# Performance work log

Hardware: AMD Instinct MI355X
Metric: run time of the kernel (lower is better)

## Reference

```python
import jax, jax.numpy as jnp
import numpy as np

B, S, D_IN, D_OUT = 4, 2048, 2048, 2048
E, R, TOP_K = 8, 8, 2
ALPHA = 16.0
SCALE = ALPHA / R  # alpha / r


def setup_inputs() -> dict:
    key = jax.random.key(0)
    ks = jax.random.split(key, 6)
    x = jax.random.normal(ks[0], (B, S, D_IN), dtype=jnp.float32)
    # base frozen linear: torch Linear weight [out, in], bias [out]
    W_base = jax.random.normal(ks[1], (D_OUT, D_IN), dtype=jnp.float32) / np.sqrt(D_IN)
    b_base = jax.random.normal(ks[2], (D_OUT,), dtype=jnp.float32) * 0.01
    # router: Linear(in_features, num_experts, bias=False) -> weight [E, in]
    W_router = jax.random.normal(ks[3], (E, D_IN), dtype=jnp.float32) / np.sqrt(D_IN)
    # LoRA experts: A [E, r, in], B [E, out, r] (torch inits B to zero; use small
    # random values so outputs/grads are non-trivial -- math is identical)
    A_w = jax.random.normal(ks[4], (E, R, D_IN), dtype=jnp.float32) / np.sqrt(D_IN)
    B_w = jax.random.normal(ks[5], (E, D_OUT, R), dtype=jnp.float32) * 0.02
    return {"x": x, "W_base": W_base, "b_base": b_base,
            "W_router": W_router, "A_w": A_w, "B_w": B_w}


def reference(x, W_base, b_base, W_router, A_w, B_w):
    # frozen base linear: [B,S,out]
    y = jnp.einsum('bsd,od->bso', x, W_base) + b_base
    # router: logits [B,S,E] -> top-k + softmax over the k selected logits
    logits = jnp.einsum('bsd,ed->bse', x, W_router)
    topk_vals, topk_idx = jax.lax.top_k(logits, TOP_K)       # [B,S,k]
    gates = jax.nn.softmax(topk_vals, axis=-1)               # [B,S,k]
    # all-experts LoRA compute (matches the original dense-stack semantics)
    h = jnp.einsum('bsd,erd->bser', x, A_w)                  # [B,S,E,r]
    expert_outs = jnp.einsum('bser,eor->bseo', h, B_w) * SCALE  # [B,S,E,out]
    # gather the top-k expert outputs and combine with gates
    topk_outs = jnp.take_along_axis(expert_outs, topk_idx[..., None], axis=2)  # [B,S,k,out]
    fused = jnp.sum(topk_outs * gates[..., None], axis=2)    # [B,S,out]
    return y + fused
```

## Files before the change

### kernel.cpp

```cpp
#include <hip/hip_runtime.h>

typedef unsigned short u16;
typedef __attribute__((ext_vector_type(8))) short short8;
typedef __attribute__((ext_vector_type(4))) float f32x4;

#define GLL16(g, l) __builtin_amdgcn_global_load_lds(                         \
    (const __attribute__((address_space(1))) void*)(g),                        \
    (__attribute__((address_space(3))) void*)(l), 16, 0, 0)

__device__ __forceinline__ u16 f2bf(float f) {
  union { float f; unsigned u; } v; v.f = f;
  unsigned u = v.u;
  return (u16)((u + 0x7FFFu + ((u >> 16) & 1u)) >> 16);
}

__global__ __launch_bounds__(512) void k_conv_router(
    const float* __restrict__ x, const float* __restrict__ Wr,
    u16* __restrict__ xbf, float* __restrict__ logits)
{
  __shared__ float wlds[16384];
  {
    const float4* src = (const float4*)Wr;
    float4* dst = (float4*)wlds;
    int t = threadIdx.x;
#pragma unroll
    for (int i = 0; i < 8; ++i) dst[t + i * 512] = src[t + i * 512];
  }
  __syncthreads();
  int wave = threadIdx.x >> 6, lane = threadIdx.x & 63;
  const float4* wv = (const float4*)wlds;
#pragma unroll 1
  for (int s = 0; s < 2; ++s) {
    int tok = blockIdx.x * 16 + wave * 2 + s;
    const float4* xrow = (const float4*)(x + tok * 2048);
    ushort4* orow = (ushort4*)(xbf + tok * 2048);
    float acc[8];
#pragma unroll
    for (int e = 0; e < 8; ++e) acc[e] = 0.f;
#pragma unroll 1
    for (int i = 0; i < 8; ++i) {
      float4 xv = xrow[lane + i * 64];
      ushort4 o;
      o.x = f2bf(xv.x); o.y = f2bf(xv.y);
      o.z = f2bf(xv.z); o.w = f2bf(xv.w);
      orow[lane + i * 64] = o;
#pragma unroll
      for (int e = 0; e < 8; ++e) {
        float4 b = wv[e * 512 + lane + i * 64];
        acc[e] += xv.x * b.x + xv.y * b.y + xv.z * b.z + xv.w * b.w;
      }
    }
#pragma unroll
    for (int e = 0; e < 8; ++e) {
      float v = acc[e];
#pragma unroll
      for (int off = 32; off > 0; off >>= 1) v += __shfl_xor(v, off, 64);
      acc[e] = v;
    }
    if (lane == 0) {
#pragma unroll
      for (int e = 0; e < 8; ++e) logits[tok * 8 + e] = acc[e];
    }
  }
}

__global__ __launch_bounds__(256) void k_convert(
    const float* __restrict__ Wb, const float* __restrict__ Aw,
    const float* __restrict__ Bw,
    u16* __restrict__ wbf, u16* __restrict__ aabf, u16* __restrict__ bmt)
{
  int b = blockIdx.x, t = threadIdx.x;
  if (b < 1024) {
    int tid = b * 256 + t;
    const float4* src = (const float4*)Wb;
    ushort4* dst = (ushort4*)wbf;
#pragma unroll
    for (int i = 0; i < 4; ++i) {
      float4 v = src[tid + i * 262144];
      ushort4 o; o.x = f2bf(v.x); o.y = f2bf(v.y); o.z = f2bf(v.z); o.w = f2bf(v.w);
      dst[tid + i * 262144] = o;
    }
  } else if (b < 1056) {
    int tid = (b - 1024) * 256 + t;
    const float4* src = (const float4*)Aw;
    ushort4* dst = (ushort4*)aabf;
#pragma unroll
    for (int i = 0; i < 4; ++i) {
      float4 v = src[tid + i * 8192];
      ushort4 o; o.x = f2bf(v.x); o.y = f2bf(v.y); o.z = f2bf(v.z); o.w = f2bf(v.w);
      dst[tid + i * 8192] = o;
    }
  } else {
    int n = (b - 1056) * 256 + t;
#pragma unroll
    for (int e = 0; e < 8; ++e) {
      const float4* src = (const float4*)(Bw + e * 16384 + n * 8);
      float4 v0 = src[0], v1 = src[1];
      ushort4 o0, o1;
      o0.x = f2bf(v0.x); o0.y = f2bf(v0.y); o0.z = f2bf(v0.z); o0.w = f2bf(v0.w);
      o1.x = f2bf(v1.x); o1.y = f2bf(v1.y); o1.z = f2bf(v1.z); o1.w = f2bf(v1.w);
      ushort4* dst = (ushort4*)(bmt + n * 64 + e * 8);
      dst[0] = o0; dst[1] = o1;
    }
  }
}

__global__ __launch_bounds__(256) void k_hgemm(
    const u16* __restrict__ xbf, const u16* __restrict__ aabf,
    float* __restrict__ P)
{
  __shared__ u16 As[256 * 64];
  __shared__ u16 Bs[64 * 64];
  int t = threadIdx.x, wave = t >> 6, lane = t & 63;
  int mBase = blockIdx.x * 256;
  int ks = blockIdx.y;
  int fr = lane & 15, fg = lane >> 4;
  int lrow = lane >> 3, lcol = (lane & 7) * 8;
  f32x4 zero = {0.f, 0.f, 0.f, 0.f};
  f32x4 acc[4][4];
#pragma unroll
  for (int i = 0; i < 4; ++i)
#pragma unroll
    for (int j = 0; j < 4; ++j) acc[i][j] = zero;
#pragma unroll 1
  for (int it = 0; it < 4; ++it) {
    int k0 = ks * 256 + it * 64;
    __syncthreads();
#pragma unroll
    for (int cc = 0; cc < 8; ++cc) {
      int c = wave * 8 + cc;
      GLL16(xbf + (mBase + c * 8 + lrow) * 2048 + k0 + lcol, &As[c * 512]);
    }
#pragma unroll
    for (int cc = 0; cc < 2; ++cc) {
      int c = wave * 2 + cc;
      GLL16(aabf + (c * 8 + lrow) * 2048 + k0 + lcol, &Bs[c * 512]);
    }
    __syncthreads();
#pragma unroll
    for (int kk = 0; kk < 2; ++kk) {
      short8 a[4], bfr[4];
#pragma unroll
      for (int i = 0; i < 4; ++i)
        a[i] = *(const short8*)&As[(wave * 64 + i * 16 + fr) * 64 + kk * 32 + fg * 8];
#pragma unroll
      for (int j = 0; j < 4; ++j)
        bfr[j] = *(const short8*)&Bs[(j * 16 + fr) * 64 + kk * 32 + fg * 8];
#pragma unroll
      for (int i = 0; i < 4; ++i)
#pragma unroll
        for (int j = 0; j < 4; ++j)
          acc[i][j] = __builtin_amdgcn_mfma_f32_16x16x32_bf16(a[i], bfr[j], acc[i][j], 0, 0, 0);
    }
  }
#pragma unroll
  for (int i = 0; i < 4; ++i)
#pragma unroll
    for (int j = 0; j < 4; ++j)
#pragma unroll
      for (int r = 0; r < 4; ++r) {
        int m = mBase + wave * 64 + i * 16 + fg * 4 + r;
        int n = j * 16 + fr;
        P[(ks * 8192 + m) * 64 + n] = acc[i][j][r];
      }
}

__global__ __launch_bounds__(256) void k_topk(
    const float* __restrict__ logits, const float* __restrict__ P,
    u16* __restrict__ G)
{
  int t = threadIdx.x, wave = t >> 6, lane = t & 63;
  int tok = blockIdx.x * 4 + wave;
  const float* lg = logits + tok * 8;
  float la[8];
#pragma unroll
  for (int e = 0; e < 8; ++e) la[e] = lg[e];
  float v0 = la[0]; int i0 = 0;
#pragma unroll
  for (int e = 1; e < 8; ++e) { if (la[e] > v0) { v0 = la[e]; i0 = e; } }
  float v1 = -3.4e38f; int i1 = 0;
#pragma unroll
  for (int e = 0; e < 8; ++e) { if (e != i0 && la[e] > v1) { v1 = la[e]; i1 = e; } }
  float ex = expf(v1 - v0);
  float inv = 1.f / (1.f + ex);
  float gate0 = inv, gate1 = ex * inv;
  int e = lane >> 3;
  float h = 0.f;
#pragma unroll
  for (int ks = 0; ks < 8; ++ks) h += P[(ks * 8192 + tok) * 64 + lane];
  float g = (e == i0) ? gate0 : ((e == i1) ? gate1 : 0.f);
  G[tok * 64 + lane] = f2bf(2.0f * g * h);
}

__global__ __launch_bounds__(512, 2) void k_main(
    const u16* __restrict__ xbf, const u16* __restrict__ wbf,
    const u16* __restrict__ G, const u16* __restrict__ BmT,
    const float* __restrict__ bias, float* __restrict__ out)
{
  __shared__ u16 lds[65536];
  const int tid = threadIdx.x;
  const int w = tid >> 6, lane = tid & 63;
  const int fr = lane & 15, fg = lane >> 4;
  const int wr = w >> 2, wc = w & 3;

  const int b0 = blockIdx.x;
  const int wg = (b0 & 7) * 32 + (b0 >> 3);
  const int mBase = (wg >> 3) * 256;
  const int nBase = (wg & 7) * 256;

  const int rl = lane >> 3;
  const int ce = ((lane & 7) ^ rl) << 3;
  const int swz = (fr & 7) << 3;
  const int colk0 = (fg * 8) ^ swz;
  const int colk1 = (32 + fg * 8) ^ swz;
  const int aOff = (wr * 128 + fr) * 64;
  const int bOff = (wc * 64 + fr) * 64;

  f32x4 acc[8][4];
  const f32x4 zero = {0.f, 0.f, 0.f, 0.f};
#pragma unroll
  for (int mi = 0; mi < 8; ++mi)
#pragma unroll
    for (int nj = 0; nj < 4; ++nj) acc[mi][nj] = zero;

  auto STAGE = [&](int s, int which) {
    if (s > 32) return;
    const bool isA = (which < 2);
    const int h = which & 1;
    const u16* src; int ld, k0;
    if (s < 32) { src = isA ? xbf : wbf; ld = 2048; k0 = s * 64; }
    else        { src = isA ? G   : BmT; ld = 64;   k0 = 0;      }
    const int rb = (isA ? mBase : nBase) + h * 128 + w * 8 + rl;
    u16* dst = lds + (isA ? 0 : 32768) + (s & 1) * 16384 + h * 8192 + w * 512;
    GLL16(src + rb * ld + k0 + ce, dst);
    GLL16(src + (rb + 64) * ld + k0 + ce, dst + 4096);
  };

#define MFMA_BURST(NJ)                                                        \
  __builtin_amdgcn_s_setprio(1);                                              \
  _Pragma("unroll")                                                           \
  for (int kk = 0; kk < 2; ++kk) {                                            \
    _Pragma("unroll")                                                         \
    for (int mi = 0; mi < 8; ++mi)                                            \
      acc[mi][NJ] = __builtin_amdgcn_mfma_f32_16x16x32_bf16(                  \
          a[mi][kk], bb[NJ][kk], acc[mi][NJ], 0, 0, 0);                       \
  }                                                                           \
  __builtin_amdgcn_s_setprio(0);

  STAGE(0, 0); STAGE(0, 1); STAGE(0, 2); STAGE(0, 3);
  STAGE(1, 0); STAGE(1, 2); STAGE(1, 1);
  asm volatile("s_waitcnt vmcnt(6)" ::: "memory");
  __builtin_amdgcn_s_barrier();

  short8 a[8][2], bb[4][2];
#pragma unroll 1
  for (int t = 0; t < 33; ++t) {
    const u16* Ab = lds + (t & 1) * 16384;
    const u16* Bb = lds + 32768 + (t & 1) * 16384;
#pragma unroll
    for (int mi = 0; mi < 8; ++mi) {
      a[mi][0] = *(const short8*)(Ab + aOff + mi * 1024 + colk0);
      a[mi][1] = *(const short8*)(Ab + aOff + mi * 1024 + colk1);
    }
#pragma unroll
    for (int nj = 0; nj < 2; ++nj) {
      bb[nj][0] = *(const short8*)(Bb + bOff + nj * 1024 + colk0);
      bb[nj][1] = *(const short8*)(Bb + bOff + nj * 1024 + colk1);
    }
    STAGE(t + 1, 3);
    __builtin_amdgcn_s_barrier();
    asm volatile("s_waitcnt lgkmcnt(0)" ::: "memory");
    MFMA_BURST(0)
    __builtin_amdgcn_s_barrier();
#pragma unroll
    for (int nj = 2; nj < 4; ++nj) {
      bb[nj][0] = *(const short8*)(Bb + bOff + nj * 1024 + colk0);
      bb[nj][1] = *(const short8*)(Bb + bOff + nj * 1024 + colk1);
    }
    STAGE(t + 2, 0);
    __builtin_amdgcn_s_barrier();
    asm volatile("s_waitcnt lgkmcnt(0)" ::: "memory");
    MFMA_BURST(1)
    __builtin_amdgcn_s_barrier();
    STAGE(t + 2, 2);
    __builtin_amdgcn_s_barrier();
    MFMA_BURST(2)
    __builtin_amdgcn_s_barrier();
    STAGE(t + 2, 1);
    __builtin_amdgcn_s_barrier();
    MFMA_BURST(3)
    if (t < 31)       { asm volatile("s_waitcnt vmcnt(6)" ::: "memory"); }
    else if (t == 31) { asm volatile("s_waitcnt vmcnt(0)" ::: "memory"); }
    __builtin_amdgcn_s_barrier();
  }

#pragma unroll
  for (int nj = 0; nj < 4; ++nj) {
    const int n = nBase + wc * 64 + nj * 16 + fr;
    const float bv = bias[n];
#pragma unroll
    for (int mi = 0; mi < 8; ++mi) {
      const int m = mBase + wr * 128 + mi * 16 + fg * 4;
#pragma unroll
      for (int r = 0; r < 4; ++r)
        out[(m + r) * 2048 + n] = acc[mi][nj][r] + bv;
    }
  }
#undef MFMA_BURST
}

extern "C" void kernel_launch(void* const* d_in, const int* in_sizes, int n_in,
                              void* d_out, int out_size, void* d_ws, size_t ws_size,
                              hipStream_t stream) {
  const float* x  = (const float*)d_in[0];
  const float* Wb = (const float*)d_in[1];
  const float* bb = (const float*)d_in[2];
  const float* Wr = (const float*)d_in[3];
  const float* Aw = (const float*)d_in[4];
  const float* Bw = (const float*)d_in[5];

  char* ws = (char*)d_ws;
  u16*   xbf  = (u16*)  (ws + 0);
  u16*   wbf  = (u16*)  (ws + 33554432);
  u16*   aabf = (u16*)  (ws + 41943040);
  u16*   bmt  = (u16*)  (ws + 42205184);
  float* lgt  = (float*)(ws + 42467328);
  u16*   G    = (u16*)  (ws + 42729472);
  float* P   = (float*)d_out;
  float* out = (float*)d_out;

  hipLaunchKernelGGL(k_conv_router, dim3(512),    dim3(512), 0, stream, x, Wr, xbf, lgt);
  hipLaunchKernelGGL(k_convert,     dim3(1064),   dim3(256), 0, stream, Wb, Aw, Bw, wbf, aabf, bmt);
  hipLaunchKernelGGL(k_hgemm,       dim3(32, 8),  dim3(256), 0, stream, xbf, aabf, P);
  hipLaunchKernelGGL(k_topk,        dim3(2048),   dim3(256), 0, stream, lgt, P, G);
  hipLaunchKernelGGL(k_main,        dim3(256),    dim3(512), 0, stream, xbf, wbf, G, bmt, bb, out);
}
```

Before: 127.0 us.

## Restructure GEMM main loop to stream A fragments per M-quad with reordered staging

After: 122.3 us. -3.7%, faster.

```diff
diff --git a/kernel.cpp b/kernel.cpp
--- a/kernel.cpp
+++ b/kernel.cpp
@@ -236,60 +236,65 @@
     GLL16(src + (rb + 64) * ld + k0 + ce, dst + 4096);
   };
 
-#define MFMA_BURST(NJ)                                                        \
+#define RDA(AV, MI0)                                                          \
+  AV[0][0] = *(const short8*)(Ab + aOff + (MI0) * 1024 + colk0);              \
+  AV[0][1] = *(const short8*)(Ab + aOff + (MI0) * 1024 + colk1);              \
+  AV[1][0] = *(const short8*)(Ab + aOff + (MI0 + 1) * 1024 + colk0);          \
+  AV[1][1] = *(const short8*)(Ab + aOff + (MI0 + 1) * 1024 + colk1);
+
+#define MFMA_QUAD(AV, MI0)                                                    \
   __builtin_amdgcn_s_setprio(1);                                              \
   _Pragma("unroll")                                                           \
-  for (int kk = 0; kk < 2; ++kk) {                                            \
+  for (int q = 0; q < 2; ++q)                                                 \
     _Pragma("unroll")                                                         \
-    for (int mi = 0; mi < 8; ++mi)                                            \
-      acc[mi][NJ] = __builtin_amdgcn_mfma_f32_16x16x32_bf16(                  \
-          a[mi][kk], bb[NJ][kk], acc[mi][NJ], 0, 0, 0);                       \
-  }                                                                           \
+    for (int nj = 0; nj < 4; ++nj)                                            \
+      _Pragma("unroll")                                                       \
+      for (int kk = 0; kk < 2; ++kk)                                          \
+        acc[MI0 + q][nj] = __builtin_amdgcn_mfma_f32_16x16x32_bf16(           \
+            AV[q][kk], bb[nj][kk], acc[MI0 + q][nj], 0, 0, 0);                \
   __builtin_amdgcn_s_setprio(0);
 
   STAGE(0, 0); STAGE(0, 1); STAGE(0, 2); STAGE(0, 3);
-  STAGE(1, 0); STAGE(1, 2); STAGE(1, 1);
-  asm volatile("s_waitcnt vmcnt(6)" ::: "memory");
+  STAGE(1, 2); STAGE(1, 3);
+  asm volatile("s_waitcnt vmcnt(4)" ::: "memory");
   __builtin_amdgcn_s_barrier();
 
-  short8 a[8][2], bb[4][2];
 #pragma unroll 1
   for (int t = 0; t < 33; ++t) {
     const u16* Ab = lds + (t & 1) * 16384;
     const u16* Bb = lds + 32768 + (t & 1) * 16384;
-#pragma unroll
-    for (int mi = 0; mi < 8; ++mi) {
-      a[mi][0] = *(const short8*)(Ab + aOff + mi * 1024 + colk0);
-      a[mi][1] = *(const short8*)(Ab + aOff + mi * 1024 + colk1);
-    }
-#pragma unroll
-    for (int nj = 0; nj < 2; ++nj) {
+    short8 bb[4][2];
+    short8 a0[2][2], a1[2][2], a2[2][2], a3[2][2];
+#pragma unroll
+    for (int nj = 0; nj < 4; ++nj) {
       bb[nj][0] = *(const short8*)(Bb + bOff + nj * 1024 + colk0);
       bb[nj][1] = *(const short8*)(Bb + bOff + nj * 1024 + colk1);
     }
-    STAGE(t + 1, 3);
+    RDA(a0, 0)
+    STAGE(t + 1, 0);
+    asm volatile("s_waitcnt lgkmcnt(8)" ::: "memory");
     __builtin_amdgcn_s_barrier();
     asm volatile("s_waitcnt lgkmcnt(0)" ::: "memory");
-    MFMA_BURST(0)
-    __builtin_amdgcn_s_barrier();
-#pragma unroll
-    for (int nj = 2; nj < 4; ++nj) {
-      bb[nj][0] = *(const short8*)(Bb + bOff + nj * 1024 + colk0);
-      bb[nj][1] = *(const short8*)(Bb + bOff + nj * 1024 + colk1);
-    }
-    STAGE(t + 2, 0);
+    MFMA_QUAD(a0, 0)
+    __builtin_amdgcn_s_barrier();
+    RDA(a1, 2)
+    STAGE(t + 1, 1);
     __builtin_amdgcn_s_barrier();
     asm volatile("s_waitcnt lgkmcnt(0)" ::: "memory");
-    MFMA_BURST(1)
-    __builtin_amdgcn_s_barrier();
+    MFMA_QUAD(a1, 2)
+    __builtin_amdgcn_s_barrier();
+    RDA(a2, 4)
     STAGE(t + 2, 2);
     __builtin_amdgcn_s_barrier();
-    MFMA_BURST(2)
-    __builtin_amdgcn_s_barrier();
-    STAGE(t + 2, 1);
-    __builtin_amdgcn_s_barrier();
-    MFMA_BURST(3)
-    if (t < 31)       { asm volatile("s_waitcnt vmcnt(6)" ::: "memory"); }
+    asm volatile("s_waitcnt lgkmcnt(0)" ::: "memory");
+    MFMA_QUAD(a2, 4)
+    __builtin_amdgcn_s_barrier();
+    RDA(a3, 6)
+    STAGE(t + 2, 3);
+    __builtin_amdgcn_s_barrier();
+    asm volatile("s_waitcnt lgkmcnt(0)" ::: "memory");
+    MFMA_QUAD(a3, 6)
+    if (t < 31)       { asm volatile("s_waitcnt vmcnt(4)" ::: "memory"); }
     else if (t == 31) { asm volatile("s_waitcnt vmcnt(0)" ::: "memory"); }
     __builtin_amdgcn_s_barrier();
   }
@@ -306,7 +311,8 @@
         out[(m + r) * 2048 + n] = acc[mi][nj][r] + bv;
     }
   }
-#undef MFMA_BURST
+#undef MFMA_QUAD
+#undef RDA
 }
 
 extern "C" void kernel_launch(void* const* d_in, const int* in_sizes, int n_in,
```

## Restructure GEMM main loop into register double-buffered 4-phase MFMA schedule

Applied to the files above, without the earlier changes.

Result: faster. 116.6 us (-8.2%).

```diff
diff --git a/kernel.cpp b/kernel.cpp
--- a/kernel.cpp
+++ b/kernel.cpp
@@ -236,62 +236,103 @@
     GLL16(src + (rb + 64) * ld + k0 + ce, dst + 4096);
   };
 
-#define MFMA_BURST(NJ)                                                        \
+  short8 Aa[2][2], Ab[2][2];
+  short8 Bx[4][2], By[4][2];
+
+#define LGKM(N) asm volatile("s_waitcnt lgkmcnt(" #N ")" ::: "memory")
+#define VMC(N)  asm volatile("s_waitcnt vmcnt(" #N ")" ::: "memory")
+#define BAR()   __builtin_amdgcn_s_barrier()
+
+#define RDA(DST, BUF, MI0)                                                    \
+  DST[0][0] = *(const short8*)((BUF) + aOff + (MI0) * 1024 + colk0);          \
+  DST[0][1] = *(const short8*)((BUF) + aOff + (MI0) * 1024 + colk1);          \
+  DST[1][0] = *(const short8*)((BUF) + aOff + ((MI0) + 1) * 1024 + colk0);    \
+  DST[1][1] = *(const short8*)((BUF) + aOff + ((MI0) + 1) * 1024 + colk1);
+
+#define RDB(DST, BUF, NJ0)                                                    \
+  DST[(NJ0)][0] = *(const short8*)((BUF) + bOff + (NJ0) * 1024 + colk0);      \
+  DST[(NJ0)][1] = *(const short8*)((BUF) + bOff + (NJ0) * 1024 + colk1);      \
+  DST[(NJ0)+1][0] = *(const short8*)((BUF) + bOff + ((NJ0)+1) * 1024 + colk0);\
+  DST[(NJ0)+1][1] = *(const short8*)((BUF) + bOff + ((NJ0)+1) * 1024 + colk1);
+
+#define MFMA16(AV, BV, MI0)                                                   \
   __builtin_amdgcn_s_setprio(1);                                              \
   _Pragma("unroll")                                                           \
-  for (int kk = 0; kk < 2; ++kk) {                                            \
+  for (int kk = 0; kk < 2; ++kk)                                              \
     _Pragma("unroll")                                                         \
-    for (int mi = 0; mi < 8; ++mi)                                            \
-      acc[mi][NJ] = __builtin_amdgcn_mfma_f32_16x16x32_bf16(                  \
-          a[mi][kk], bb[NJ][kk], acc[mi][NJ], 0, 0, 0);                       \
-  }                                                                           \
+    for (int q = 0; q < 2; ++q)                                               \
+      _Pragma("unroll")                                                       \
+      for (int nj = 0; nj < 4; ++nj)                                          \
+        acc[(MI0) + q][nj] = __builtin_amdgcn_mfma_f32_16x16x32_bf16(         \
+            AV[q][kk], BV[nj][kk], acc[(MI0) + q][nj], 0, 0, 0);              \
   __builtin_amdgcn_s_setprio(0);
 
+#define TILE(T, P, BC, BN)                                                    \
+  {                                                                           \
+    const u16* Acur = lds + (P) * 16384;                                      \
+    const u16* Anxt = lds + (1 - (P)) * 16384;                                \
+    const u16* Bnxt = lds + 32768 + (1 - (P)) * 16384;                        \
+                                                                      \
+    STAGE((T) + 1, 0);                                                        \
+    RDA(Ab, Acur, 2)                                                          \
+    LGKM(4);                                                                  \
+    MFMA16(Aa, BC, 0)                                                         \
+    BAR();                                                                    \
+                                                                      \
+    STAGE((T) + 1, 1);                                                        \
+    RDA(Aa, Acur, 4)                                                          \
+    LGKM(4);                                                                  \
+    MFMA16(Ab, BC, 2)                                                         \
+    VMC(4);                                                                   \
+    BAR();                                                                    \
+                                                                      \
+    STAGE((T) + 2, 2);                                                        \
+    RDA(Ab, Acur, 6)                                                          \
+    RDB(BN, Bnxt, 0)                                                          \
+    LGKM(8);                                                                  \
+    MFMA16(Aa, BC, 4)                                                         \
+    if ((T) == 31) { VMC(0); } else { VMC(2); }                               \
+    BAR();                                                                    \
+                                                                      \
+    STAGE((T) + 2, 3);                                                        \
+    RDA(Aa, Anxt, 0)                                                          \
+    RDB(BN, Bnxt, 2)                                                          \
+    LGKM(8);                                                                  \
+    MFMA16(Ab, BC, 6)                                                         \
+    BAR();                                                                    \
+  }
+
   STAGE(0, 0); STAGE(0, 1); STAGE(0, 2); STAGE(0, 3);
-  STAGE(1, 0); STAGE(1, 2); STAGE(1, 1);
-  asm volatile("s_waitcnt vmcnt(6)" ::: "memory");
-  __builtin_amdgcn_s_barrier();
-
-  short8 a[8][2], bb[4][2];
+  STAGE(1, 2); STAGE(1, 3);
+  VMC(4);
+  BAR();
+  {
+    const u16* Bb0 = lds + 32768;
+    RDB(Bx, Bb0, 0)
+    RDB(Bx, Bb0, 2)
+    RDA(Aa, lds, 0)
+  }
+
 #pragma unroll 1
-  for (int t = 0; t < 33; ++t) {
-    const u16* Ab = lds + (t & 1) * 16384;
-    const u16* Bb = lds + 32768 + (t & 1) * 16384;
-#pragma unroll
-    for (int mi = 0; mi < 8; ++mi) {
-      a[mi][0] = *(const short8*)(Ab + aOff + mi * 1024 + colk0);
-      a[mi][1] = *(const short8*)(Ab + aOff + mi * 1024 + colk1);
-    }
-#pragma unroll
-    for (int nj = 0; nj < 2; ++nj) {
-      bb[nj][0] = *(const short8*)(Bb + bOff + nj * 1024 + colk0);
-      bb[nj][1] = *(const short8*)(Bb + bOff + nj * 1024 + colk1);
-    }
-    STAGE(t + 1, 3);
-    __builtin_amdgcn_s_barrier();
-    asm volatile("s_waitcnt lgkmcnt(0)" ::: "memory");
-    MFMA_BURST(0)
-    __builtin_amdgcn_s_barrier();
-#pragma unroll
-    for (int nj = 2; nj < 4; ++nj) {
-      bb[nj][0] = *(const short8*)(Bb + bOff + nj * 1024 + colk0);
-      bb[nj][1] = *(const short8*)(Bb + bOff + nj * 1024 + colk1);
-    }
-    STAGE(t + 2, 0);
-    __builtin_amdgcn_s_barrier();
-    asm volatile("s_waitcnt lgkmcnt(0)" ::: "memory");
-    MFMA_BURST(1)
-    __builtin_amdgcn_s_barrier();
-    STAGE(t + 2, 2);
-    __builtin_amdgcn_s_barrier();
-    MFMA_BURST(2)
-    __builtin_amdgcn_s_barrier();
-    STAGE(t + 2, 1);
-    __builtin_amdgcn_s_barrier();
-    MFMA_BURST(3)
-    if (t < 31)       { asm volatile("s_waitcnt vmcnt(6)" ::: "memory"); }
-    else if (t == 31) { asm volatile("s_waitcnt vmcnt(0)" ::: "memory"); }
-    __builtin_amdgcn_s_barrier();
+  for (int tt = 0; tt < 16; ++tt) {
+    const int t0 = tt * 2;
+    TILE(t0, 0, Bx, By)
+    TILE(t0 + 1, 1, By, Bx)
+  }
+
+  {
+    const u16* Acur = lds;
+    RDA(Ab, Acur, 2)
+    LGKM(4);
+    MFMA16(Aa, Bx, 0)
+    RDA(Aa, Acur, 4)
+    LGKM(4);
+    MFMA16(Ab, Bx, 2)
+    RDA(Ab, Acur, 6)
+    LGKM(4);
+    MFMA16(Aa, Bx, 4)
+    LGKM(0);
+    MFMA16(Ab, Bx, 6)
   }
 
 #pragma unroll
@@ -306,7 +347,13 @@
         out[(m + r) * 2048 + n] = acc[mi][nj][r] + bv;
     }
   }
-#undef MFMA_BURST
+#undef TILE
+#undef MFMA16
+#undef RDB
+#undef RDA
+#undef BAR
+#undef VMC
+#undef LGKM
 }
 
 extern "C" void kernel_launch(void* const* d_in, const int* in_sizes, int n_in,
```

## Restructure main GEMM loop into quadrant MFMA phases with split A fragment loads

Applied to the files above, without the earlier changes.

After: 121.7 us. -4.2%, faster.

```diff
diff --git a/kernel.cpp b/kernel.cpp
--- a/kernel.cpp
+++ b/kernel.cpp
@@ -236,62 +236,71 @@
     GLL16(src + (rb + 64) * ld + k0 + ce, dst + 4096);
   };
 
-#define MFMA_BURST(NJ)                                                        \
+#define LGKM(N) asm volatile("s_waitcnt lgkmcnt(" #N ")" ::: "memory")
+#define VMC(N)  asm volatile("s_waitcnt vmcnt(" #N ")" ::: "memory")
+#define BAR()   __builtin_amdgcn_s_barrier()
+
+#define RDA4(DST, BUF, MI0)                                                   \
+  _Pragma("unroll")                                                           \
+  for (int q = 0; q < 4; ++q) {                                               \
+    DST[q][0] = *(const short8*)((BUF) + aOff + ((MI0) + q) * 1024 + colk0);  \
+    DST[q][1] = *(const short8*)((BUF) + aOff + ((MI0) + q) * 1024 + colk1);  \
+  }
+
+#define RDB2(NJ0)                                                             \
+  Bv[(NJ0)][0]     = *(const short8*)(Bbuf + bOff + (NJ0) * 1024 + colk0);    \
+  Bv[(NJ0)][1]     = *(const short8*)(Bbuf + bOff + (NJ0) * 1024 + colk1);    \
+  Bv[(NJ0) + 1][0] = *(const short8*)(Bbuf + bOff + ((NJ0)+1) * 1024 + colk0);\
+  Bv[(NJ0) + 1][1] = *(const short8*)(Bbuf + bOff + ((NJ0)+1) * 1024 + colk1);
+
+#define MFMAQ(AV, ACCB, NJ0)                                                  \
   __builtin_amdgcn_s_setprio(1);                                              \
   _Pragma("unroll")                                                           \
-  for (int kk = 0; kk < 2; ++kk) {                                            \
+  for (int kk = 0; kk < 2; ++kk)                                              \
     _Pragma("unroll")                                                         \
-    for (int mi = 0; mi < 8; ++mi)                                            \
-      acc[mi][NJ] = __builtin_amdgcn_mfma_f32_16x16x32_bf16(                  \
-          a[mi][kk], bb[NJ][kk], acc[mi][NJ], 0, 0, 0);                       \
-  }                                                                           \
+    for (int q = 0; q < 4; ++q)                                               \
+      _Pragma("unroll")                                                       \
+      for (int nj = 0; nj < 2; ++nj)                                          \
+        acc[(ACCB) + q][(NJ0) + nj] =                                         \
+            __builtin_amdgcn_mfma_f32_16x16x32_bf16(                          \
+                AV[q][kk], Bv[(NJ0) + nj][kk],                                \
+                acc[(ACCB) + q][(NJ0) + nj], 0, 0, 0);                        \
   __builtin_amdgcn_s_setprio(0);
 
-  STAGE(0, 0); STAGE(0, 1); STAGE(0, 2); STAGE(0, 3);
-  STAGE(1, 0); STAGE(1, 2); STAGE(1, 1);
-  asm volatile("s_waitcnt vmcnt(6)" ::: "memory");
-  __builtin_amdgcn_s_barrier();
-
-  short8 a[8][2], bb[4][2];
+  STAGE(0, 2); STAGE(0, 3); STAGE(0, 0); STAGE(0, 1);
+  STAGE(1, 2); STAGE(1, 3); STAGE(1, 0); STAGE(1, 1);
+  VMC(8);
+  BAR();
+
 #pragma unroll 1
   for (int t = 0; t < 33; ++t) {
-    const u16* Ab = lds + (t & 1) * 16384;
-    const u16* Bb = lds + 32768 + (t & 1) * 16384;
-#pragma unroll
-    for (int mi = 0; mi < 8; ++mi) {
-      a[mi][0] = *(const short8*)(Ab + aOff + mi * 1024 + colk0);
-      a[mi][1] = *(const short8*)(Ab + aOff + mi * 1024 + colk1);
-    }
-#pragma unroll
-    for (int nj = 0; nj < 2; ++nj) {
-      bb[nj][0] = *(const short8*)(Bb + bOff + nj * 1024 + colk0);
-      bb[nj][1] = *(const short8*)(Bb + bOff + nj * 1024 + colk1);
-    }
-    STAGE(t + 1, 3);
-    __builtin_amdgcn_s_barrier();
-    asm volatile("s_waitcnt lgkmcnt(0)" ::: "memory");
-    MFMA_BURST(0)
-    __builtin_amdgcn_s_barrier();
-#pragma unroll
-    for (int nj = 2; nj < 4; ++nj) {
-      bb[nj][0] = *(const short8*)(Bb + bOff + nj * 1024 + colk0);
-      bb[nj][1] = *(const short8*)(Bb + bOff + nj * 1024 + colk1);
-    }
-    STAGE(t + 2, 0);
-    __builtin_amdgcn_s_barrier();
-    asm volatile("s_waitcnt lgkmcnt(0)" ::: "memory");
-    MFMA_BURST(1)
-    __builtin_amdgcn_s_barrier();
-    STAGE(t + 2, 2);
-    __builtin_amdgcn_s_barrier();
-    MFMA_BURST(2)
-    __builtin_amdgcn_s_barrier();
-    STAGE(t + 2, 1);
-    __builtin_amdgcn_s_barrier();
-    MFMA_BURST(3)
-    if (t < 31)       { asm volatile("s_waitcnt vmcnt(6)" ::: "memory"); }
-    else if (t == 31) { asm volatile("s_waitcnt vmcnt(0)" ::: "memory"); }
-    __builtin_amdgcn_s_barrier();
+    const u16* Abuf = lds + (t & 1) * 16384;
+    const u16* Bbuf = lds + 32768 + (t & 1) * 16384;
+    short8 A03[4][2], A47[4][2], Bv[4][2];
+    RDA4(A03, Abuf, 0)
+    RDB2(0)
+    LGKM(8);
+    BAR();
+    LGKM(0);
+    MFMAQ(A03, 0, 0)
+    BAR();
+    RDB2(2)
+    BAR();
+    LGKM(0);
+    MFMAQ(A03, 0, 2)
+    BAR();
+    RDA4(A47, Abuf, 4)
+    STAGE(t + 2, 2); STAGE(t + 2, 3);
+    BAR();
+    LGKM(0);
+    MFMAQ(A47, 4, 0)
+    BAR();
+    STAGE(t + 2, 0); STAGE(t + 2, 1);
+    BAR();
+    MFMAQ(A47, 4, 2)
+    if (t < 31)       { VMC(6); }
+    else if (t == 31) { VMC(0); }
+    BAR();
   }
 
 #pragma unroll
@@ -306,7 +315,12 @@
         out[(m + r) * 2048 + n] = acc[mi][nj][r] + bv;
     }
   }
-#undef MFMA_BURST
+#undef MFMAQ
+#undef RDB2
+#undef RDA4
+#undef BAR
+#undef VMC
+#undef LGKM
 }
 
 extern "C" void kernel_launch(void* const* d_in, const int* in_sizes, int n_in,
@@ -329,9 +343,9 @@
   float* P   = (float*)d_out;
   float* out = (float*)d_out;
 
-  hipLaunchKernelGGL(k_conv_router, dim3(512),    dim3(512), 0, stream, x, Wr, xbf, lgt);
-  hipLaunchKernelGGL(k_convert,     dim3(1064),   dim3(256), 0, stream, Wb, Aw, Bw, wbf, aabf, bmt);
-  hipLaunchKernelGGL(k_hgemm,       dim3(32, 8),  dim3(256), 0, stream, xbf, aabf, P);
-  hipLaunchKernelGGL(k_topk,        dim3(2048),   dim3(256), 0, stream, lgt, P, G);
-  hipLaunchKernelGGL(k_main,        dim3(256),    dim3(512), 0, stream, xbf, wbf, G, bmt, bb, out);
-}
+  hipLaunchKernelGGL(k_conv_router, dim3(512),   dim3(512), 0, stream, x, Wr, xbf, lgt);
+  hipLaunchKernelGGL(k_convert,     dim3(1064),  dim3(256), 0, stream, Wb, Aw, Bw, wbf, aabf, bmt);
+  hipLaunchKernelGGL(k_hgemm,       dim3(32, 8), dim3(256), 0, stream, xbf, aabf, P);
+  hipLaunchKernelGGL(k_topk,        dim3(2048),  dim3(256), 0, stream, lgt, P, G);
+  hipLaunchKernelGGL(k_main,        dim3(256),   dim3(512), 0, stream, xbf, wbf, G, bmt, bb, out);
+}
```
